# Optimization experiments

Hardware: AMD Instinct MI355X
Metric: run time of the kernel (lower is better)

The kernel has to match this reference:

```python
import jax, jax.numpy as jnp
import numpy as np

B, D_IN, H, D_OUT = 4096, 4096, 2048, 1000
LN_EPS = 1e-5


def setup_inputs() -> dict:
    key = jax.random.key(0)
    ks = jax.random.split(key, 8)
    s_in = 1.0 / np.sqrt(H)  # torch RNN init: U(-1/sqrt(H), 1/sqrt(H))
    inp = {
        "x": jax.random.normal(ks[0], (B, D_IN), dtype=jnp.float32),
        "W_ih0": jax.random.uniform(ks[1], (H, D_IN), jnp.float32, -s_in, s_in),
        "b_ih0": jax.random.uniform(ks[2], (H,), jnp.float32, -s_in, s_in),
        "b_hh0": jax.random.uniform(ks[3], (H,), jnp.float32, -s_in, s_in),
        "W_ih1": jax.random.uniform(ks[4], (H, H), jnp.float32, -s_in, s_in),
        "b_ih1": jax.random.uniform(ks[5], (H,), jnp.float32, -s_in, s_in),
        "b_hh1": jax.random.uniform(ks[6], (H,), jnp.float32, -s_in, s_in),
        "ln_g": jnp.ones((2 * H,), jnp.float32),
        "ln_b": jnp.zeros((2 * H,), jnp.float32),
        "fc_W": jax.random.uniform(ks[7], (D_OUT, 2 * H), jnp.float32, -1.0 / np.sqrt(2 * H), 1.0 / np.sqrt(2 * H)),
        "fc_b": jnp.zeros((D_OUT,), jnp.float32),
    }
    return inp


def reference(x, W_ih0, b_ih0, b_hh0, W_ih1, b_ih1, b_hh1, ln_g, ln_b, fc_W, fc_b):
    # seq_len == 1, h0 == 0 -> W_hh terms vanish; only biases remain.
    h1 = jnp.tanh(x @ W_ih0.T + b_ih0 + b_hh0)          # [B, H]
    h2 = jnp.tanh(h1 @ W_ih1.T + b_ih1 + b_hh1)         # [B, H]
    # last_hidden == mean_pooled (single step) -> concat duplicates h2
    combined = jnp.concatenate([h2, h2], axis=1)        # [B, 2H]
    mu = combined.mean(axis=-1, keepdims=True)
    var = combined.var(axis=-1, keepdims=True)
    normed = (combined - mu) * jax.lax.rsqrt(var + LN_EPS) * ln_g + ln_b
    # dropout is identity in eval mode
    return normed @ fc_W.T + fc_b                        # [B, D_OUT]
```

## Files before the change

### kernel.cpp

```cpp
#include <hip/hip_runtime.h>
#include <hip/hip_bf16.h>

typedef __attribute__((ext_vector_type(8))) unsigned short ushort8;
typedef __attribute__((ext_vector_type(8))) __bf16 bf16x8;
typedef __attribute__((ext_vector_type(4))) float f32x4;
typedef __attribute__((ext_vector_type(4))) float floatx4;

__device__ __forceinline__ unsigned short f2bf(float f) {
    unsigned u = __builtin_bit_cast(unsigned, f);
    u += 0x7fffu + ((u >> 16) & 1u);
    return (unsigned short)(u >> 16);
}
__device__ __forceinline__ float bf2f(unsigned short h) {
    unsigned u = ((unsigned)h) << 16;
    return __builtin_bit_cast(float, u);
}

__device__ __forceinline__ void gload_lds16(const void* g, void* l) {
    __builtin_amdgcn_global_load_lds(
        (const __attribute__((address_space(1))) void*)g,
        (__attribute__((address_space(3))) void*)l,
        16, 0, 0);
}

#define BAR()   asm volatile("s_barrier" ::: "memory")
#define VMW0()  asm volatile("s_waitcnt vmcnt(0)" ::: "memory")
#define LGK0()  asm volatile("s_waitcnt lgkmcnt(0)" ::: "memory")
#define SGB_DS(n)   __builtin_amdgcn_sched_group_barrier(0x100, n, 0)
#define SGB_MFMA(n) __builtin_amdgcn_sched_group_barrier(0x008, n, 0)

__global__ __launch_bounds__(256) void cvt_f2bf(const float* __restrict__ in,
                                                unsigned short* __restrict__ out,
                                                int n8) {
    int i = blockIdx.x * 256 + threadIdx.x;
    if (i >= n8) return;
    floatx4 a = ((const floatx4*)in)[2 * i];
    floatx4 b = ((const floatx4*)in)[2 * i + 1];
    ushort8 o;
#pragma unroll
    for (int j = 0; j < 4; ++j) { o[j] = f2bf(a[j]); o[4 + j] = f2bf(b[j]); }
    ((ushort8*)out)[i] = o;
}

__global__ __launch_bounds__(256) void weff_kernel(const float* __restrict__ fcW,
                                                   const float* __restrict__ lng,
                                                   const float* __restrict__ lnb,
                                                   const float* __restrict__ fcb,
                                                   unsigned short* __restrict__ weff,
                                                   float* __restrict__ cc,
                                                   float* __restrict__ wsum) {
    int o = blockIdx.x;
    int tid = threadIdx.x;
    if (o >= 1000) {
        ushort8 z = {0, 0, 0, 0, 0, 0, 0, 0};
        ((ushort8*)(weff + (size_t)o * 2048))[tid] = z;
        if (tid == 0) { cc[o] = 0.f; wsum[o] = 0.f; }
        return;
    }
    const float* wrow = fcW + (size_t)o * 4096;
    int j0 = tid * 8;
    floatx4 wa  = *(const floatx4*)(wrow + j0);
    floatx4 wb  = *(const floatx4*)(wrow + j0 + 4);
    floatx4 wa2 = *(const floatx4*)(wrow + 2048 + j0);
    floatx4 wb2 = *(const floatx4*)(wrow + 2048 + j0 + 4);
    floatx4 ga  = *(const floatx4*)(lng + j0);
    floatx4 gb  = *(const floatx4*)(lng + j0 + 4);
    floatx4 ga2 = *(const floatx4*)(lng + 2048 + j0);
    floatx4 gb2 = *(const floatx4*)(lng + 2048 + j0 + 4);
    floatx4 ba  = *(const floatx4*)(lnb + j0);
    floatx4 bb  = *(const floatx4*)(lnb + j0 + 4);
    floatx4 ba2 = *(const floatx4*)(lnb + 2048 + j0);
    floatx4 bb2 = *(const floatx4*)(lnb + 2048 + j0 + 4);
    ushort8 o8;
    float acc = 0.f, ws = 0.f;
#pragma unroll
    for (int j = 0; j < 4; ++j) {
        o8[j] = f2bf(ga[j] * wa[j] + ga2[j] * wa2[j]);
        acc += ba[j] * wa[j] + ba2[j] * wa2[j];
        ws  += bf2f(o8[j]);
        o8[4 + j] = f2bf(gb[j] * wb[j] + gb2[j] * wb2[j]);
        acc += bb[j] * wb[j] + bb2[j] * wb2[j];
        ws  += bf2f(o8[4 + j]);
    }
    ((ushort8*)(weff + (size_t)o * 2048))[tid] = o8;
#pragma unroll
    for (int d = 32; d; d >>= 1) { acc += __shfl_down(acc, d); ws += __shfl_down(ws, d); }
    __shared__ float red[4], redw[4];
    if ((tid & 63) == 0) { red[tid >> 6] = acc; redw[tid >> 6] = ws; }
    __syncthreads();
    if (tid == 0) {
        cc[o] = fcb[o] + red[0] + red[1] + red[2] + red[3];
        wsum[o] = redw[0] + redw[1] + redw[2] + redw[3];
    }
}

__global__ __launch_bounds__(256) void ln_stats(const unsigned short* __restrict__ h2,
                                                float2* __restrict__ mur) {
    int row = blockIdx.x, tid = threadIdx.x;
    ushort8 v = ((const ushort8*)(h2 + (size_t)row * 2048))[tid];
    float s = 0.f, s2 = 0.f;
#pragma unroll
    for (int j = 0; j < 8; ++j) { float f = bf2f(v[j]); s += f; s2 += f * f; }
#pragma unroll
    for (int d = 32; d; d >>= 1) { s += __shfl_down(s, d); s2 += __shfl_down(s2, d); }
    __shared__ float rs_[4], rs2_[4];
    if ((tid & 63) == 0) { rs_[tid >> 6] = s; rs2_[tid >> 6] = s2; }
    __syncthreads();
    if (tid == 0) {
        float S = rs_[0] + rs_[1] + rs_[2] + rs_[3];
        float S2 = rs2_[0] + rs2_[1] + rs2_[2] + rs2_[3];
        float mu = S * (1.f / 2048.f);
        float var = S2 * (1.f / 2048.f) - mu * mu;
        mur[row] = make_float2(mu, rsqrtf(var + 1e-5f));
    }
}

__global__ __launch_bounds__(256) void reduce_tanh(const unsigned short* __restrict__ P0,
                                                   const unsigned short* __restrict__ P1,
                                                   const float* __restrict__ b0,
                                                   const float* __restrict__ b1,
                                                   unsigned short* __restrict__ out) {
    int i = blockIdx.x * 256 + threadIdx.x;
    ushort8 p0 = ((const ushort8*)P0)[i];
    ushort8 p1 = ((const ushort8*)P1)[i];
    int c0 = (i * 8) & 2047;
    floatx4 ba = *(const floatx4*)(b0 + c0), bb = *(const floatx4*)(b0 + c0 + 4);
    floatx4 ca = *(const floatx4*)(b1 + c0), cb = *(const floatx4*)(b1 + c0 + 4);
    ushort8 o;
#pragma unroll
    for (int j = 0; j < 4; ++j) {
        o[j]     = f2bf(tanhf(bf2f(p0[j])     + bf2f(p1[j])     + ba[j] + ca[j]));
        o[4 + j] = f2bf(tanhf(bf2f(p0[4 + j]) + bf2f(p1[4 + j]) + bb[j] + cb[j]));
    }
    ((ushort8*)out)[i] = o;
}

__global__ __launch_bounds__(512, 2) void gemm256i(const unsigned short* __restrict__ A,
                                                   const unsigned short* __restrict__ B,
                                                   int Ks, int KP, int N,
                                                   unsigned short* __restrict__ Pa,
                                                   unsigned short* __restrict__ Pb) {
    extern __shared__ char smem[];
    const int tid = threadIdx.x;
    const int lane = tid & 63;
    const int wid = tid >> 6;
    const int wm = wid >> 2, wn = wid & 3;
    const int fr = lane & 15, g = lane >> 4;
    const int kp = blockIdx.z;

    const int gx = gridDim.x;
    const int nwg = gx * gridDim.y;
    const int fid = blockIdx.y * gx + blockIdx.x;
    const int cpx = nwg >> 3;
    const int sw = (fid & 7) * cpx + (fid >> 3);
    const int bx = sw % gx, by = sw / gx;
    const int row0 = by * 256, col0 = bx * 256;
    const int kbase = kp * KP;

    const int srow = tid >> 2;
    const int scole = ((tid & 3) ^ ((tid >> 3) & 3)) << 3;
    auto stage = [&](int kt, char* buf) {
        const size_t koff = (size_t)(kbase + kt * 32 + scole);
#pragma unroll
        for (int r = 0; r < 2; ++r)
            gload_lds16(A + (size_t)(row0 + r * 128 + srow) * Ks + koff,
                        buf + r * 8192 + tid * 16);
#pragma unroll
        for (int r = 0; r < 2; ++r)
            gload_lds16(B + (size_t)(col0 + r * 128 + srow) * Ks + koff,
                        buf + 16384 + r * 8192 + tid * 16);
    };

    const int kb = (g * 16) ^ (((fr >> 1) & 3) << 4);
    const char* pA0 = smem + (wm * 128 + fr) * 64 + kb;
    const char* pB0 = smem + 16384 + (wn * 64 + fr) * 64 + kb;
    const char* pA1 = pA0 + 32768;
    const char* pB1 = pB0 + 32768;

#define LDF(p, off) __builtin_bit_cast(bf16x8, *(const ushort8*)((p) + (off)))
#define MF4(aC, bC, mm) \
    acc[mm][0] = __builtin_amdgcn_mfma_f32_16x16x32_bf16(aC[mm], bC[0], acc[mm][0], 0, 0, 0); \
    acc[mm][1] = __builtin_amdgcn_mfma_f32_16x16x32_bf16(aC[mm], bC[1], acc[mm][1], 0, 0, 0); \
    acc[mm][2] = __builtin_amdgcn_mfma_f32_16x16x32_bf16(aC[mm], bC[2], acc[mm][2], 0, 0, 0); \
    acc[mm][3] = __builtin_amdgcn_mfma_f32_16x16x32_bf16(aC[mm], bC[3], acc[mm][3], 0, 0, 0);
#define SGBCHAIN() \
    SGB_DS(2); SGB_MFMA(4); SGB_DS(2); SGB_MFMA(4); SGB_DS(2); SGB_MFMA(4); \
    SGB_DS(2); SGB_MFMA(4); SGB_DS(2); SGB_MFMA(4); SGB_DS(2); SGB_MFMA(4); \
    SGB_MFMA(4); SGB_MFMA(4);
#define TILE_BODY(aC, bC, aN, bN, pAn, pBn) do { \
    bN[0] = LDF(pBn, 0);    bN[1] = LDF(pBn, 1024); \
    MF4(aC, bC, 0); \
    bN[2] = LDF(pBn, 2048); bN[3] = LDF(pBn, 3072); \
    MF4(aC, bC, 1); \
    aN[0] = LDF(pAn, 0);    aN[1] = LDF(pAn, 1024); \
    MF4(aC, bC, 2); \
    aN[2] = LDF(pAn, 2048); aN[3] = LDF(pAn, 3072); \
    MF4(aC, bC, 3); \
    aN[4] = LDF(pAn, 4096); aN[5] = LDF(pAn, 5120); \
    MF4(aC, bC, 4); \
    aN[6] = LDF(pAn, 6144); aN[7] = LDF(pAn, 7168); \
    MF4(aC, bC, 5); \
    MF4(aC, bC, 6); \
    MF4(aC, bC, 7); \
    SGBCHAIN(); \
} while (0)

    f32x4 acc[8][4];
#pragma unroll
    for (int i = 0; i < 8; ++i)
#pragma unroll
        for (int j = 0; j < 4; ++j) acc[i][j] = f32x4{0.f, 0.f, 0.f, 0.f};

    bf16x8 aX[8], bX[4], aY[8], bY[4];

    stage(0, smem);
    stage(1, smem + 32768);
    asm volatile("s_waitcnt vmcnt(4)" ::: "memory");
    BAR();
#pragma unroll
    for (int n = 0; n < 4; ++n) bX[n] = LDF(pB0, n * 1024);
#pragma unroll
    for (int m = 0; m < 8; ++m) aX[m] = LDF(pA0, m * 1024);

    const int NT = KP >> 5;
    for (int t = 0; t < NT - 2; t += 2) {
        LGK0(); VMW0(); BAR();
        stage(t + 2, smem);
        TILE_BODY(aX, bX, aY, bY, pA1, pB1);
        LGK0(); VMW0(); BAR();
        stage(t + 3, smem + 32768);
        TILE_BODY(aY, bY, aX, bX, pA0, pB0);
    }
    LGK0(); VMW0(); BAR();
    TILE_BODY(aX, bX, aY, bY, pA1, pB1);
#pragma unroll
    for (int m = 0; m < 8; ++m) { MF4(aY, bY, m); }

    unsigned short* P = kp ? Pb : Pa;
#pragma unroll
    for (int m = 0; m < 8; ++m) {
        int rbase = row0 + wm * 128 + m * 16 + g * 4;
#pragma unroll
        for (int n = 0; n < 4; ++n) {
            int col = col0 + wn * 64 + n * 16 + fr;
#pragma unroll
            for (int r = 0; r < 4; ++r)
                P[(size_t)(rbase + r) * N + col] = f2bf(acc[m][n][r]);
        }
    }
#undef TILE_BODY
#undef SGBCHAIN
#undef MF4
#undef LDF
}

template <int EPI, int NJ>
__global__ __launch_bounds__(512, 2) void gemm_rp(const unsigned short* __restrict__ A,
                                                  const unsigned short* __restrict__ B,
                                                  int M, int N, int K,
                                                  const float* __restrict__ bias0,
                                                  const float* __restrict__ bias1,
                                                  void* __restrict__ Cout, int ncols,
                                                  const float2* __restrict__ mur,
                                                  const float* __restrict__ wsum) {
    extern __shared__ char smem[];
    constexpr int BUFSZ = 16384 + NJ * 8192;
    const int tid = threadIdx.x;
    const int lane = tid & 63, wid = tid >> 6;
    const int wm = wid >> 2, wn = wid & 3;
    const int fr = lane & 15, g = lane >> 4;

    const int nwg = gridDim.x * gridDim.y;
    const int fid = blockIdx.y * gridDim.x + blockIdx.x;
    const int cpx = nwg >> 3;
    const int sw = (fid & 7) * cpx + (fid >> 3);
    const int bx = sw % gridDim.x, by = sw / gridDim.x;
    const int row0 = by * 128, col0 = bx * (64 * NJ);

    const int tg = tid >> 3;
    const int tcE = ((tid & 7) ^ (tg & 7)) * 8;

    auto stage = [&](int kt, char* buf) {
#pragma unroll
        for (int r = 0; r < 2; ++r)
            gload_lds16(A + (size_t)(row0 + r * 64 + tg) * K + kt * 64 + tcE,
                        buf + r * 8192 + wid * 1024);
#pragma unroll
        for (int rr = 0; rr < NJ; ++rr)
            gload_lds16(B + (size_t)(col0 + rr * 64 + tg) * K + kt * 64 + tcE,
                        buf + 16384 + rr * 8192 + wid * 1024);
    };

    const int xorv = (fr & 7) << 4;
    auto readFrags = [&](bf16x8 (&fa)[4][2], bf16x8 (&fb)[NJ][2], const char* buf) {
#pragma unroll
        for (int m = 0; m < 4; ++m)
#pragma unroll
            for (int kh = 0; kh < 2; ++kh)
                fa[m][kh] = __builtin_bit_cast(bf16x8, *(const ushort8*)(
                    buf + (wm * 64 + m * 16 + fr) * 128 + ((kh * 64 + g * 16) ^ xorv)));
#pragma unroll
        for (int n = 0; n < NJ; ++n)
#pragma unroll
            for (int kh = 0; kh < 2; ++kh)
                fb[n][kh] = __builtin_bit_cast(bf16x8, *(const ushort8*)(
                    buf + 16384 + (wn * (16 * NJ) + n * 16 + fr) * 128 + ((kh * 64 + g * 16) ^ xorv)));
    };

    f32x4 acc[4][NJ];
#pragma unroll
    for (int i = 0; i < 4; ++i)
#pragma unroll
        for (int j = 0; j < NJ; ++j) acc[i][j] = f32x4{0.f, 0.f, 0.f, 0.f};

    auto domfma = [&](bf16x8 (&fa)[4][2], bf16x8 (&fb)[NJ][2]) {
        __builtin_amdgcn_s_setprio(1);
#pragma unroll
        for (int m = 0; m < 4; ++m)
#pragma unroll
            for (int n = 0; n < NJ; ++n)
#pragma unroll
                for (int kh = 0; kh < 2; ++kh)
                    acc[m][n] = __builtin_amdgcn_mfma_f32_16x16x32_bf16(fa[m][kh], fb[n][kh], acc[m][n], 0, 0, 0);
        __builtin_amdgcn_s_setprio(0);
    };

    bf16x8 aX[4][2], bX[NJ][2], aY[4][2], bY[NJ][2];

    stage(0, smem); stage(1, smem + BUFSZ);
    if constexpr (NJ == 4) { asm volatile("s_waitcnt vmcnt(6)" ::: "memory"); }
    else                   { asm volatile("s_waitcnt vmcnt(4)" ::: "memory"); }
    BAR();
    readFrags(aX, bX, smem);

    const int NT = K >> 6;
    for (int t = 0; t < NT; t += 2) {
        if (t + 2 < NT) {
            stage(t + 2, smem + ((t + 2) % 3) * BUFSZ);
            if constexpr (NJ == 4) { asm volatile("s_waitcnt vmcnt(6)" ::: "memory"); }
            else                   { asm volatile("s_waitcnt vmcnt(4)" ::: "memory"); }
        } else {
            VMW0();
        }
        BAR();
        readFrags(aY, bY, smem + ((t + 1) % 3) * BUFSZ);
        domfma(aX, bX);

        if (t + 2 < NT) {
            if (t + 3 < NT) {
                stage(t + 3, smem + ((t + 3) % 3) * BUFSZ);
                if constexpr (NJ == 4) { asm volatile("s_waitcnt vmcnt(6)" ::: "memory"); }
                else                   { asm volatile("s_waitcnt vmcnt(4)" ::: "memory"); }
            } else {
                VMW0();
            }
            BAR();
            readFrags(aX, bX, smem + ((t + 2) % 3) * BUFSZ);
        }
        domfma(aY, bY);
    }

#pragma unroll
    for (int i = 0; i < 4; ++i) {
        int rbase = row0 + wm * 64 + i * 16 + g * 4;
        if (EPI == 0) {
#pragma unroll
            for (int j = 0; j < NJ; ++j) {
                int col = col0 + wn * (16 * NJ) + j * 16 + fr;
                float bsum = bias0[col] + bias1[col];
                unsigned short* O = (unsigned short*)Cout;
#pragma unroll
                for (int r = 0; r < 4; ++r)
                    O[(size_t)(rbase + r) * N + col] = f2bf(tanhf(acc[i][j][r] + bsum));
            }
        } else {
            float2 mr[4];
#pragma unroll
            for (int r = 0; r < 4; ++r) mr[r] = mur[rbase + r];
#pragma unroll
            for (int j = 0; j < NJ; ++j) {
                int col = col0 + wn * (16 * NJ) + j * 16 + fr;
                if (col < ncols) {
                    float ws = wsum[col];
                    float ccv = bias0[col];
                    float* O = (float*)Cout;
#pragma unroll
                    for (int r = 0; r < 4; ++r)
                        O[(size_t)(rbase + r) * ncols + col] =
                            mr[r].y * (acc[i][j][r] - mr[r].x * ws) + ccv;
                }
            }
        }
    }
}

extern "C" void kernel_launch(void* const* d_in, const int* in_sizes, int n_in,
                              void* d_out, int out_size, void* d_ws, size_t ws_size,
                              hipStream_t stream) {
    const float* x   = (const float*)d_in[0];
    const float* W0  = (const float*)d_in[1];
    const float* bi0 = (const float*)d_in[2];
    const float* bh0 = (const float*)d_in[3];
    const float* W1  = (const float*)d_in[4];
    const float* bi1 = (const float*)d_in[5];
    const float* bh1 = (const float*)d_in[6];
    const float* lng = (const float*)d_in[7];
    const float* lnb = (const float*)d_in[8];
    const float* fcW = (const float*)d_in[9];
    const float* fcb = (const float*)d_in[10];
    float* out = (float*)d_out;

    char* w = (char*)d_ws;
    unsigned short* xb   = (unsigned short*)(w);
    unsigned short* w0b  = (unsigned short*)(w + 33554432ull);
    unsigned short* w1b  = (unsigned short*)(w + 50331648ull);
    unsigned short* h1   = (unsigned short*)(w + 58720256ull);
    unsigned short* h2   = (unsigned short*)(w + 75497472ull);
    unsigned short* weff = (unsigned short*)(w + 92274688ull);
    float* cc            = (float*)(w + 96468992ull);
    float* wsum          = (float*)(w + 96473088ull);
    float2* mur          = (float2*)(w + 96477184ull);
    unsigned short* P1a  = h2;
    unsigned short* P1b  = (unsigned short*)(w + 96509952ull);
    unsigned short* P2a  = xb;
    unsigned short* P2b  = (unsigned short*)(w + 16777216ull);

    const int SHM256 = 65536;
    const int SHM1 = 3 * (16384 + 2 * 8192);
    (void)hipFuncSetAttribute((const void*)gemm256i,
                              hipFuncAttributeMaxDynamicSharedMemorySize, SHM256);
    (void)hipFuncSetAttribute((const void*)gemm_rp<1, 2>,
                              hipFuncAttributeMaxDynamicSharedMemorySize, SHM1);

    cvt_f2bf<<<8192, 256, 0, stream>>>(x,  xb,  2097152);
    cvt_f2bf<<<4096, 256, 0, stream>>>(W0, w0b, 1048576);
    cvt_f2bf<<<2048, 256, 0, stream>>>(W1, w1b, 524288);
    weff_kernel<<<1024, 256, 0, stream>>>(fcW, lng, lnb, fcb, weff, cc, wsum);

    gemm256i<<<dim3(8, 16, 2), 512, SHM256, stream>>>(xb, w0b, 4096, 2048, 2048, P1a, P1b);
    reduce_tanh<<<4096, 256, 0, stream>>>(P1a, P1b, bi0, bh0, h1);

    gemm256i<<<dim3(8, 16, 2), 512, SHM256, stream>>>(h1, w1b, 2048, 1024, 2048, P2a, P2b);
    reduce_tanh<<<4096, 256, 0, stream>>>(P2a, P2b, bi1, bh1, h2);

    ln_stats<<<4096, 256, 0, stream>>>(h2, mur);
    gemm_rp<1, 2><<<dim3(8, 32), 512, SHM1, stream>>>(h2, weff, 4096, 1024, 2048,
                                                      cc, nullptr, out, 1000, mur, wsum);
}
```

Before: 188.6 us.

## Replace 256x256 register-pipelined GEMM with 128x256 triple-buffered LDS kernel

Swaps the split-K GEMM for the two RNN layers from a 256x256 tile with double-buffered LDS and register-level fragment prefetch to a 128x256 tile with three LDS buffers and partial vmcnt waits. The grid doubles to 8x32x2 and launch bounds ask for 4 blocks per CU, aiming for more resident waves to hide latency instead of hand-scheduled MFMA/DS interleaving. It also sets s_setprio around the MFMA block. Smaller tiles give less data reuse per block and drop the explicit instruction-schedule hints, which may lower MFMA throughput.

```diff
diff --git a/kernel.cpp b/kernel.cpp
--- a/kernel.cpp
+++ b/kernel.cpp
@@ -24,10 +24,8 @@
 }
 
 #define BAR()   asm volatile("s_barrier" ::: "memory")
+#define VMW3()  asm volatile("s_waitcnt vmcnt(3)" ::: "memory")
 #define VMW0()  asm volatile("s_waitcnt vmcnt(0)" ::: "memory")
-#define LGK0()  asm volatile("s_waitcnt lgkmcnt(0)" ::: "memory")
-#define SGB_DS(n)   __builtin_amdgcn_sched_group_barrier(0x100, n, 0)
-#define SGB_MFMA(n) __builtin_amdgcn_sched_group_barrier(0x008, n, 0)
 
 __global__ __launch_bounds__(256) void cvt_f2bf(const float* __restrict__ in,
                                                 unsigned short* __restrict__ out,
@@ -135,15 +133,15 @@
     ((ushort8*)out)[i] = o;
 }
 
-__global__ __launch_bounds__(512, 2) void gemm256i(const unsigned short* __restrict__ A,
-                                                   const unsigned short* __restrict__ B,
-                                                   int Ks, int KP, int N,
-                                                   unsigned short* __restrict__ Pa,
-                                                   unsigned short* __restrict__ Pb) {
+__global__ __launch_bounds__(512, 4) void gemm_fs(const unsigned short* __restrict__ A,
+                                                  const unsigned short* __restrict__ B,
+                                                  int Ks, int KP, int N,
+                                                  unsigned short* __restrict__ Pa,
+                                                  unsigned short* __restrict__ Pb) {
     extern __shared__ char smem[];
+    constexpr int BUFSZ = 24576;
     const int tid = threadIdx.x;
-    const int lane = tid & 63;
-    const int wid = tid >> 6;
+    const int lane = tid & 63, wid = tid >> 6;
     const int wm = wid >> 2, wn = wid & 3;
     const int fr = lane & 15, g = lane >> 4;
     const int kp = blockIdx.z;
@@ -154,92 +152,65 @@
     const int cpx = nwg >> 3;
     const int sw = (fid & 7) * cpx + (fid >> 3);
     const int bx = sw % gx, by = sw / gx;
-    const int row0 = by * 256, col0 = bx * 256;
+    const int row0 = by * 128, col0 = bx * 256;
     const int kbase = kp * KP;
 
     const int srow = tid >> 2;
-    const int scole = ((tid & 3) ^ ((tid >> 3) & 3)) << 3;
+    const int scolE = ((tid & 3) ^ ((tid >> 3) & 3)) * 8;
     auto stage = [&](int kt, char* buf) {
-        const size_t koff = (size_t)(kbase + kt * 32 + scole);
-#pragma unroll
-        for (int r = 0; r < 2; ++r)
-            gload_lds16(A + (size_t)(row0 + r * 128 + srow) * Ks + koff,
-                        buf + r * 8192 + tid * 16);
-#pragma unroll
-        for (int r = 0; r < 2; ++r)
-            gload_lds16(B + (size_t)(col0 + r * 128 + srow) * Ks + koff,
-                        buf + 16384 + r * 8192 + tid * 16);
+        const size_t koff = (size_t)(kbase + kt * 32 + scolE);
+        gload_lds16(A + (size_t)(row0 + srow) * Ks + koff, buf + tid * 16);
+#pragma unroll
+        for (int gg = 0; gg < 2; ++gg)
+            gload_lds16(B + (size_t)(col0 + gg * 128 + srow) * Ks + koff,
+                        buf + 8192 + gg * 8192 + tid * 16);
     };
 
-    const int kb = (g * 16) ^ (((fr >> 1) & 3) << 4);
-    const char* pA0 = smem + (wm * 128 + fr) * 64 + kb;
-    const char* pB0 = smem + 16384 + (wn * 64 + fr) * 64 + kb;
-    const char* pA1 = pA0 + 32768;
-    const char* pB1 = pB0 + 32768;
-
-#define LDF(p, off) __builtin_bit_cast(bf16x8, *(const ushort8*)((p) + (off)))
-#define MF4(aC, bC, mm) \
-    acc[mm][0] = __builtin_amdgcn_mfma_f32_16x16x32_bf16(aC[mm], bC[0], acc[mm][0], 0, 0, 0); \
-    acc[mm][1] = __builtin_amdgcn_mfma_f32_16x16x32_bf16(aC[mm], bC[1], acc[mm][1], 0, 0, 0); \
-    acc[mm][2] = __builtin_amdgcn_mfma_f32_16x16x32_bf16(aC[mm], bC[2], acc[mm][2], 0, 0, 0); \
-    acc[mm][3] = __builtin_amdgcn_mfma_f32_16x16x32_bf16(aC[mm], bC[3], acc[mm][3], 0, 0, 0);
-#define SGBCHAIN() \
-    SGB_DS(2); SGB_MFMA(4); SGB_DS(2); SGB_MFMA(4); SGB_DS(2); SGB_MFMA(4); \
-    SGB_DS(2); SGB_MFMA(4); SGB_DS(2); SGB_MFMA(4); SGB_DS(2); SGB_MFMA(4); \
-    SGB_MFMA(4); SGB_MFMA(4);
-#define TILE_BODY(aC, bC, aN, bN, pAn, pBn) do { \
-    bN[0] = LDF(pBn, 0);    bN[1] = LDF(pBn, 1024); \
-    MF4(aC, bC, 0); \
-    bN[2] = LDF(pBn, 2048); bN[3] = LDF(pBn, 3072); \
-    MF4(aC, bC, 1); \
-    aN[0] = LDF(pAn, 0);    aN[1] = LDF(pAn, 1024); \
-    MF4(aC, bC, 2); \
-    aN[2] = LDF(pAn, 2048); aN[3] = LDF(pAn, 3072); \
-    MF4(aC, bC, 3); \
-    aN[4] = LDF(pAn, 4096); aN[5] = LDF(pAn, 5120); \
-    MF4(aC, bC, 4); \
-    aN[6] = LDF(pAn, 6144); aN[7] = LDF(pAn, 7168); \
-    MF4(aC, bC, 5); \
-    MF4(aC, bC, 6); \
-    MF4(aC, bC, 7); \
-    SGBCHAIN(); \
-} while (0)
-
-    f32x4 acc[8][4];
-#pragma unroll
-    for (int i = 0; i < 8; ++i)
+    const int kb = (g ^ ((fr >> 1) & 3)) * 16;
+
+#define LDF(p) __builtin_bit_cast(bf16x8, *(const ushort8*)(p))
+
+    f32x4 acc[4][4];
+#pragma unroll
+    for (int i = 0; i < 4; ++i)
 #pragma unroll
         for (int j = 0; j < 4; ++j) acc[i][j] = f32x4{0.f, 0.f, 0.f, 0.f};
 
-    bf16x8 aX[8], bX[4], aY[8], bY[4];
-
-    stage(0, smem);
-    stage(1, smem + 32768);
-    asm volatile("s_waitcnt vmcnt(4)" ::: "memory");
-    BAR();
-#pragma unroll
-    for (int n = 0; n < 4; ++n) bX[n] = LDF(pB0, n * 1024);
-#pragma unroll
-    for (int m = 0; m < 8; ++m) aX[m] = LDF(pA0, m * 1024);
+    char* p0 = smem;
+    char* p1 = smem + BUFSZ;
+    char* p2 = smem + 2 * BUFSZ;
+
+    stage(0, p0); stage(1, p1);
 
     const int NT = KP >> 5;
-    for (int t = 0; t < NT - 2; t += 2) {
-        LGK0(); VMW0(); BAR();
-        stage(t + 2, smem);
-        TILE_BODY(aX, bX, aY, bY, pA1, pB1);
-        LGK0(); VMW0(); BAR();
-        stage(t + 3, smem + 32768);
-        TILE_BODY(aY, bY, aX, bX, pA0, pB0);
-    }
-    LGK0(); VMW0(); BAR();
-    TILE_BODY(aX, bX, aY, bY, pA1, pB1);
-#pragma unroll
-    for (int m = 0; m < 8; ++m) { MF4(aY, bY, m); }
+    for (int t = 0; t < NT; ++t) {
+        if (t < NT - 1) { VMW3(); } else { VMW0(); }
+        BAR();
+        if (t + 2 < NT) stage(t + 2, p2);
+
+        bf16x8 aF[4], bF[4];
+#pragma unroll
+        for (int m = 0; m < 4; ++m)
+            aF[m] = LDF(p0 + (wm * 64 + m * 16 + fr) * 64 + kb);
+#pragma unroll
+        for (int n = 0; n < 4; ++n)
+            bF[n] = LDF(p0 + 8192 + (wn * 64 + n * 16 + fr) * 64 + kb);
+
+        __builtin_amdgcn_s_setprio(1);
+#pragma unroll
+        for (int m = 0; m < 4; ++m)
+#pragma unroll
+            for (int n = 0; n < 4; ++n)
+                acc[m][n] = __builtin_amdgcn_mfma_f32_16x16x32_bf16(aF[m], bF[n], acc[m][n], 0, 0, 0);
+        __builtin_amdgcn_s_setprio(0);
+
+        char* tmp = p0; p0 = p1; p1 = p2; p2 = tmp;
+    }
 
     unsigned short* P = kp ? Pb : Pa;
 #pragma unroll
-    for (int m = 0; m < 8; ++m) {
-        int rbase = row0 + wm * 128 + m * 16 + g * 4;
+    for (int m = 0; m < 4; ++m) {
+        int rbase = row0 + wm * 64 + m * 16 + g * 4;
 #pragma unroll
         for (int n = 0; n < 4; ++n) {
             int col = col0 + wn * 64 + n * 16 + fr;
@@ -248,9 +219,6 @@
                 P[(size_t)(rbase + r) * N + col] = f2bf(acc[m][n][r]);
         }
     }
-#undef TILE_BODY
-#undef SGBCHAIN
-#undef MF4
 #undef LDF
 }
 
@@ -425,10 +393,10 @@
     unsigned short* P2a  = xb;
     unsigned short* P2b  = (unsigned short*)(w + 16777216ull);
 
-    const int SHM256 = 65536;
+    const int SHMF = 73728;
     const int SHM1 = 3 * (16384 + 2 * 8192);
-    (void)hipFuncSetAttribute((const void*)gemm256i,
-                              hipFuncAttributeMaxDynamicSharedMemorySize, SHM256);
+    (void)hipFuncSetAttribute((const void*)gemm_fs,
+                              hipFuncAttributeMaxDynamicSharedMemorySize, SHMF);
     (void)hipFuncSetAttribute((const void*)gemm_rp<1, 2>,
                               hipFuncAttributeMaxDynamicSharedMemorySize, SHM1);
 
@@ -437,10 +405,10 @@
     cvt_f2bf<<<2048, 256, 0, stream>>>(W1, w1b, 524288);
     weff_kernel<<<1024, 256, 0, stream>>>(fcW, lng, lnb, fcb, weff, cc, wsum);
 
-    gemm256i<<<dim3(8, 16, 2), 512, SHM256, stream>>>(xb, w0b, 4096, 2048, 2048, P1a, P1b);
+    gemm_fs<<<dim3(8, 32, 2), 512, SHMF, stream>>>(xb, w0b, 4096, 2048, 2048, P1a, P1b);
     reduce_tanh<<<4096, 256, 0, stream>>>(P1a, P1b, bi0, bh0, h1);
 
-    gemm256i<<<dim3(8, 16, 2), 512, SHM256, stream>>>(h1, w1b, 2048, 1024, 2048, P2a, P2b);
+    gemm_fs<<<dim3(8, 32, 2), 512, SHMF, stream>>>(h1, w1b, 2048, 1024, 2048, P2a, P2b);
     reduce_tanh<<<4096, 256, 0, stream>>>(P2a, P2b, bi1, bh1, h2);
 
     ln_stats<<<4096, 256, 0, stream>>>(h2, mur);
```

New measurement: 192.0 us. No clear change (+1.8%).
